# Optimization experiments

Hardware: AMD Instinct MI355X
Metric: run time of the kernel (lower is better)

## Reference

```python
import jax, jax.numpy as jnp
from jax import lax
import numpy as np

EPS = 1e-5
NH = 16  # attention heads (c // 16 with c = 256)


def _qconv(x, mod, phase, padding=0, groups=1):
    """Quaternion conv: real weight = modulus * cos(phase), applied per quaternion component.
    x: (B, C, Q, H, W) -> (B, O, Q, H, W)"""
    w = mod * jnp.cos(phase)
    B, C, Qd, H, W = x.shape
    xr = jnp.transpose(x, (0, 2, 1, 3, 4)).reshape(B * Qd, C, H, W)
    y = lax.conv_general_dilated(xr, w, (1, 1), [(padding, padding)] * 2,
                                 dimension_numbers=('NCHW', 'OIHW', 'NCHW'),
                                 feature_group_count=groups)
    O, Ho, Wo = y.shape[1], y.shape[2], y.shape[3]
    return jnp.transpose(y.reshape(B, Qd, O, Ho, Wo), (0, 2, 1, 3, 4))


def _bn(x):
    # IQBN/VQBN: per-channel normalization over (batch, quaternion, spatial), no affine
    m = x.mean(axis=(0, 2, 3, 4), keepdims=True)
    v = x.var(axis=(0, 2, 3, 4), keepdims=True)
    return (x - m) * lax.rsqrt(v + EPS)


def _attn(x, qkv_m, qkv_p, aproj_m, aproj_p, pe_m, pe_p):
    # QAttention: per-component multi-head self-attention over spatial tokens
    B, C, Qd, H, W = x.shape
    kd = C // NH
    qkv = _qconv(x, qkv_m, qkv_p)  # (B, 3C, Q, H, W)
    q, k, v = jnp.split(qkv, 3, axis=1)
    q = q.reshape(B, NH, kd, Qd, H * W)
    k = k.reshape(B, NH, kd, Qd, H * W)
    v = v.reshape(B, NH, kd, Qd, H * W)
    scores = jnp.einsum('bhcqn,bhcqm->bhqnm', q, k) * (kd ** -0.5)
    a = jax.nn.softmax(scores, axis=-1)
    out = jnp.einsum('bhqnm,bhdqm->bhdqn', a, v).reshape(B, C, Qd, H, W)
    # proj + depthwise positional conv on the input
    return _qconv(out, aproj_m, aproj_p) + _qconv(x, pe_m, pe_p, padding=1, groups=C)


def _psa(x, qkv_m, qkv_p, aproj_m, aproj_p, pe_m, pe_p, ffn1_m, ffn1_p, ffn2_m, ffn2_p):
    a = _attn(x, qkv_m, qkv_p, aproj_m, aproj_p, pe_m, pe_p) + x  # attn shortcut
    h = jax.nn.relu(_bn(_qconv(a, ffn1_m, ffn1_p)))
    f = _bn(_qconv(h, ffn2_m, ffn2_p))
    return f + a  # ffn shortcut


def _msab(x, guide, ec_m, ec_p, gl_w, gl_b, mproj_m, mproj_p):
    # MaxSigmoidAttnBlock (nh=1): global sigmoid gate per (batch, quaternion component)
    B, C, Qd, H, W = x.shape
    e = jax.nn.relu(_bn(_qconv(x, ec_m, ec_p)))  # (B, ec, Q, H, W)
    g = guide @ gl_w.T + gl_b                     # (B, ec)
    ec = g.shape[-1]
    a = jnp.einsum('bcqhw,bc->bq', e, g) / jnp.sqrt(jnp.asarray(ec * H * W, jnp.float32))
    a = jax.nn.sigmoid(a)  # scale param = 1.0 (scale=False)
    e = e * a[:, None, :, None, None]
    return jax.nn.relu(_bn(_qconv(e, mproj_m, mproj_p, padding=1)))


def _forward(x, guide, cv1_m, cv1_p, qkv_m, qkv_p, aproj_m, aproj_p, pe_m, pe_p,
             ffn1_m, ffn1_p, ffn2_m, ffn2_p, ec_m, ec_p, gl_w, gl_b,
             mproj_m, mproj_p, cv2_m, cv2_p):
    y = jax.nn.relu(_bn(_qconv(x, cv1_m, cv1_p)))       # (B, 2c, Q, H, W)
    a, b = jnp.split(y, 2, axis=1)                       # each (B, c, Q, H, W)
    p = _psa(b, qkv_m, qkv_p, aproj_m, aproj_p, pe_m, pe_p,
             ffn1_m, ffn1_p, ffn2_m, ffn2_p)
    m = _msab(p, guide, ec_m, ec_p, gl_w, gl_b, mproj_m, mproj_p)
    cat = jnp.concatenate([a, b, p, m], axis=1)          # (B, 4c, Q, H, W)
    return jax.nn.relu(_bn(_qconv(cat, cv2_m, cv2_p)))   # (B, c2, Q, H, W)


def setup_inputs():
    B, C1, Qd, H, W = 2, 512, 4, 24, 24
    c = 256; ecd = 128; gc = 512; C2 = 512
    ks = jax.random.split(jax.random.key(0), 24)
    def rp(k, shape, s=0.02):
        return s * jax.random.normal(k, shape, dtype=jnp.float32)
    return {
        'x': jax.random.normal(ks[0], (B, C1, Qd, H, W), dtype=jnp.float32),
        'guide': jax.random.normal(ks[1], (B, gc), dtype=jnp.float32),
        'cv1_m': rp(ks[2], (2 * c, C1, 1, 1)),
        'cv1_p': rp(ks[3], (2 * c, C1, 1, 1), 0.1),
        'qkv_m': rp(ks[4], (3 * c, c, 1, 1)),
        'qkv_p': rp(ks[5], (3 * c, c, 1, 1), 0.1),
        'aproj_m': rp(ks[6], (c, c, 1, 1)),
        'aproj_p': rp(ks[7], (c, c, 1, 1), 0.1),
        'pe_m': rp(ks[8], (c, 1, 3, 3)),
        'pe_p': rp(ks[9], (c, 1, 3, 3), 0.1),
        'ffn1_m': rp(ks[10], (2 * c, c, 1, 1)),
        'ffn1_p': rp(ks[11], (2 * c, c, 1, 1), 0.1),
        'ffn2_m': rp(ks[12], (c, 2 * c, 1, 1)),
        'ffn2_p': rp(ks[13], (c, 2 * c, 1, 1), 0.1),
        'ec_m': rp(ks[14], (ecd, c, 1, 1)),
        'ec_p': rp(ks[15], (ecd, c, 1, 1), 0.1),
        'gl_w': rp(ks[16], (ecd, gc), 0.05),
        'gl_b': jnp.zeros((ecd,), dtype=jnp.float32),
        'mproj_m': rp(ks[17], (c, ecd, 3, 3)),
        'mproj_p': rp(ks[18], (c, ecd, 3, 3), 0.1),
        'cv2_m': rp(ks[19], (C2, 4 * c, 1, 1)),
        'cv2_p': rp(ks[20], (C2, 4 * c, 1, 1), 0.1),
    }


def reference(x, guide, cv1_m, cv1_p, qkv_m, qkv_p, aproj_m, aproj_p, pe_m, pe_p,
              ffn1_m, ffn1_p, ffn2_m, ffn2_p, ec_m, ec_p, gl_w, gl_b,
              mproj_m, mproj_p, cv2_m, cv2_p):
    return _forward(x, guide, cv1_m, cv1_p, qkv_m, qkv_p, aproj_m, aproj_p, pe_m, pe_p,
                    ffn1_m, ffn1_p, ffn2_m, ffn2_p, ec_m, ec_p, gl_w, gl_b,
                    mproj_m, mproj_p, cv2_m, cv2_p)
```

## Files before the change

kernel.cpp:

```cpp
#include <hip/hip_runtime.h>
#include <math.h>

typedef __bf16 bf16x8 __attribute__((ext_vector_type(8)));
typedef float f32x4 __attribute__((ext_vector_type(4)));
typedef unsigned short u16;
typedef unsigned int u32;

__device__ __forceinline__ u16 f2bf(float f) {
  u32 u = __float_as_uint(f);
  u32 r = u + 0x7FFF + ((u >> 16) & 1);
  return (u16)(r >> 16);
}
__device__ __forceinline__ float bf2f(u16 h) { return __uint_as_float(((u32)h) << 16); }

static constexpr size_t OB_WBF = 0;
static constexpr size_t OB_WPE = 3276800;
static constexpr size_t OB_ST  = 3286016;
static constexpr size_t OB_GV  = 3310592;
static constexpr size_t OB_GACC= 3311616;
static constexpr size_t OB_CAT = 3311872;
static constexpr size_t OB_YA  = OB_CAT + 9437184;
static constexpr size_t OB_U1  = OB_YA + 9437184;
static constexpr size_t OB_U2  = OB_U1 + 4718592;
static constexpr size_t OB_U3  = OB_U2 + 14155776;
static constexpr size_t OB_AOB = OB_U3 + 4718592;
static constexpr size_t OB_A1B = OB_AOB + 2359296;
static constexpr size_t WS_TOTAL = OB_A1B + 2359296;

struct WPrepP {
  const float* m[8]; const float* p[8];
  u16* out; const float* pem; const float* pep; float* peout;
  int cum[9];
};
__global__ __launch_bounds__(256) void k_wprep(WPrepP P) {
  int i = blockIdx.x * 256 + threadIdx.x;
  if (i < 2304) P.peout[i] = P.pem[i] * cosf(P.pep[i]);
  if (i >= P.cum[8]) return;
  int s = 0;
  while (s < 7 && i >= P.cum[s + 1]) s++;
  int j = i - P.cum[s];
  int src = j;
  if (s == 6) {
    int o = j / 1152, r = j % 1152, kk = r >> 7, cc = r & 127;
    src = (o * 128 + cc) * 9 + kk;
  }
  P.out[i] = f2bf(P.m[s][src] * cosf(P.p[s][src]));
}

__global__ __launch_bounds__(256) void k_xpose(const float* x, u16* xb) {
  int bid = blockIdx.x;
  int mt = bid % 18; bid /= 18;
  int ct = bid % 16; bid /= 16;
  int q = bid & 3, b = bid >> 2;
  __shared__ float tile[32][33];
  int tj = threadIdx.x & 31, ti = threadIdx.x >> 5;
  const float* xp = x + (((size_t)(b * 512 + ct * 32) * 4 + q) * 576) + mt * 32;
#pragma unroll
  for (int ii = 0; ii < 4; ii++)
    tile[ti + ii * 8][tj] = xp[(size_t)(ti + ii * 8) * 4 * 576 + tj];
  __syncthreads();
  u16* yp = xb + ((size_t)b * 2304 + q * 576 + mt * 32) * 512 + ct * 32;
#pragma unroll
  for (int mm = 0; mm < 4; mm++)
    yp[(size_t)(mm * 8 + ti) * 512 + tj] = f2bf(tile[tj][mm * 8 + ti]);
}

struct GemmP {
  const u16* W; const u16* X; float* Y; const float* Add; u16* Yb; float* St;
  long long xOff[8];
  int lda, O, K, M, G;
};

template <int BM, int NWO, int WO, int WM>
__global__ __launch_bounds__(256) void k_gemm(GemmP P) {
  constexpr int FO = WO / 16, FM = WM / 16;
  __shared__ __align__(16) char lds[16384 + BM * 128];
  const int mt = P.M / BM;
  const int ot = P.O >> 7;
  int bid = blockIdx.x;
  const int g = bid / (mt * ot);
  const int rr = bid % (mt * ot);
  const int ob = (rr / mt) << 7;
  const int mb = (rr % mt) * BM;
  const int t = threadIdx.x, lane = t & 63, wave = t >> 6;
  const int wo = (wave % NWO) * WO, wm = (wave / NWO) * WM;
  const u16* Wp = P.W + (size_t)ob * P.K;
  const u16* Xp = P.X + P.xOff[g] + (size_t)mb * P.lda;

  f32x4 acc[FO][FM] = {};

  for (int k0 = 0; k0 < P.K; k0 += 64) {
#pragma unroll
    for (int i = 0; i < 4; i++) {
      int s = (i * 4 + wave) * 64 + lane;
      int row = s >> 3;
      int kg = (s & 7) ^ (row & 7);
      const u16* src = Wp + (size_t)row * P.K + k0 + kg * 8;
      __builtin_amdgcn_global_load_lds(
          (const __attribute__((address_space(1))) u32*)src,
          (__attribute__((address_space(3))) u32*)(lds + (size_t)(i * 4 + wave) * 1024),
          16, 0, 0);
    }
#pragma unroll
    for (int i = 0; i < BM * 8 / 256; i++) {
      int s = (i * 4 + wave) * 64 + lane;
      int row = s >> 3;
      int kg = (s & 7) ^ (row & 7);
      const u16* src = Xp + (size_t)row * P.lda + k0 + kg * 8;
      __builtin_amdgcn_global_load_lds(
          (const __attribute__((address_space(1))) u32*)src,
          (__attribute__((address_space(3))) u32*)(lds + 16384 + (size_t)(i * 4 + wave) * 1024),
          16, 0, 0);
    }
    __syncthreads();
#pragma unroll
    for (int kk = 0; kk < 2; kk++) {
      int kgl = kk * 4 + (lane >> 4);
      bf16x8 af[FO], bfm[FM];
#pragma unroll
      for (int fo = 0; fo < FO; fo++) {
        int row = wo + fo * 16 + (lane & 15);
        af[fo] = *(bf16x8*)&lds[((row << 3) + (kgl ^ (row & 7))) << 4];
      }
#pragma unroll
      for (int fm = 0; fm < FM; fm++) {
        int row = wm + fm * 16 + (lane & 15);
        bfm[fm] = *(bf16x8*)&lds[16384 + (((row << 3) + (kgl ^ (row & 7))) << 4)];
      }
#pragma unroll
      for (int fo = 0; fo < FO; fo++)
#pragma unroll
        for (int fm = 0; fm < FM; fm++)
          acc[fo][fm] = __builtin_amdgcn_mfma_f32_16x16x32_bf16(af[fo], bfm[fm], acc[fo][fm], 0, 0, 0);
    }
    __syncthreads();
  }

  size_t ybase = (size_t)g * P.M * P.O;
#pragma unroll
  for (int fo = 0; fo < FO; fo++) {
    int ow = ob + wo + fo * 16 + ((lane >> 4) << 2);
#pragma unroll
    for (int fm = 0; fm < FM; fm++) {
      int m = mb + wm + fm * 16 + (lane & 15);
      f32x4 v = acc[fo][fm];
      size_t off = ybase + (size_t)m * P.O + ow;
      if (P.Add) v += *(const f32x4*)&P.Add[off];
      if (P.Y) *(f32x4*)&P.Y[off] = v;
      if (P.Yb) {
        ushort4 r;
        r.x = f2bf(v[0]); r.y = f2bf(v[1]); r.z = f2bf(v[2]); r.w = f2bf(v[3]);
        *(ushort4*)&P.Yb[off] = r;
      }
    }
  }

  if (P.St) {
#pragma unroll
    for (int fo = 0; fo < FO; fo++) {
      float sv[4], qv[4];
#pragma unroll
      for (int j = 0; j < 4; j++) { sv[j] = 0.f; qv[j] = 0.f; }
#pragma unroll
      for (int fm = 0; fm < FM; fm++)
#pragma unroll
        for (int j = 0; j < 4; j++) {
          float a = acc[fo][fm][j];
          sv[j] += a;
          qv[j] = fmaf(a, a, qv[j]);
        }
#pragma unroll
      for (int j = 0; j < 4; j++) {
#pragma unroll
        for (int mk = 1; mk < 16; mk <<= 1) {
          sv[j] += __shfl_xor(sv[j], mk, 64);
          qv[j] += __shfl_xor(qv[j], mk, 64);
        }
      }
      if ((lane & 15) == 0) {
        int o = ob + wo + fo * 16 + ((lane >> 4) << 2);
#pragma unroll
        for (int j = 0; j < 4; j++) {
          atomicAdd(&P.St[2 * (o + j)], sv[j]);
          atomicAdd(&P.St[2 * (o + j) + 1], qv[j]);
        }
      }
    }
  }
}

struct NormP {
  const float* X; const float* st; const float* Add;
  u16* Yb; float* Yf; const float* gv; float* gacc;
  long long ybOff[8];
  int ldyb, O, G, M, relu;
  float n;
};
__global__ __launch_bounds__(256) void k_norm(NormP P) {
  int O4 = P.O >> 2;
  long long idx = (long long)blockIdx.x * 256 + threadIdx.x;
  if (idx >= (long long)P.G * P.M * O4) return;
  int c4 = (int)(idx % O4);
  long long gm = idx / O4;
  int m = (int)(gm % P.M);
  int g = (int)(gm / P.M);
  size_t off = (size_t)gm * P.O + c4 * 4;
  f32x4 v = *(const f32x4*)&P.X[off];
  float inv_n = 1.0f / P.n;
#pragma unroll
  for (int j = 0; j < 4; j++) {
    int c = c4 * 4 + j;
    float mean = P.st[2 * c] * inv_n;
    float var = P.st[2 * c + 1] * inv_n - mean * mean;
    v[j] = (v[j] - mean) * rsqrtf(var + 1e-5f);
  }
  if (P.Add) v += *(const f32x4*)&P.Add[off];
  if (P.relu) {
#pragma unroll
    for (int j = 0; j < 4; j++) v[j] = fmaxf(v[j], 0.f);
  }
  if (P.Yb) {
    ushort4 r;
    r.x = f2bf(v[0]); r.y = f2bf(v[1]); r.z = f2bf(v[2]); r.w = f2bf(v[3]);
    *(ushort4*)(P.Yb + P.ybOff[g] + (size_t)m * P.ldyb + c4 * 4) = r;
  }
  if (P.Yf) *(f32x4*)&P.Yf[off] = v;
  if (P.gacc) {
    float gs = 0.f;
#pragma unroll
    for (int j = 0; j < 4; j++) gs = fmaf(v[j], P.gv[g * 128 + c4 * 4 + j], gs);
#pragma unroll
    for (int mk = 1; mk < 64; mk <<= 1) gs += __shfl_xor(gs, mk, 64);
    __shared__ float t1[4];
    int lane = threadIdx.x & 63, wv = threadIdx.x >> 6;
    if (lane == 0) t1[wv] = gs;
    __syncthreads();
    if (threadIdx.x == 0)
      atomicAdd(&P.gacc[g * 4 + m / 576], t1[0] + t1[1] + t1[2] + t1[3]);
  }
}

__global__ __launch_bounds__(256) void k_normT(const float* X, const float* st, float* out) {
  int idx = blockIdx.x * 256 + threadIdx.x;
  if (idx >= 2 * 512 * 576) return;
  int m4 = idx % 576;
  int bo = idx / 576;
  int o = bo & 511, b = bo >> 9;
  float inv_n = 1.0f / 4608.0f;
  float mean = st[2 * o] * inv_n;
  float var = st[2 * o + 1] * inv_n - mean * mean;
  float rs = rsqrtf(var + 1e-5f);
  f32x4 v;
#pragma unroll
  for (int j = 0; j < 4; j++) {
    float x = X[((size_t)b * 2304 + m4 * 4 + j) * 512 + o];
    v[j] = fmaxf((x - mean) * rs, 0.f);
  }
  *(f32x4*)&out[(size_t)bo * 2304 + m4 * 4] = v;
}

__global__ __launch_bounds__(256) void k_pe(const u16* catb, const float* wpe, float* rf) {
  int idx = blockIdx.x * 256 + threadIdx.x;
  if (idx >= 2 * 2304 * 64) return;
  int c4 = idx & 63;
  int gm = idx >> 6;
  int m = gm % 2304, g = gm / 2304;
  int q = m / 576, hw = m % 576, h = hw / 24, w = hw % 24;
  const u16* base = catb + (size_t)g * 2304 * 1024 + 256 + c4 * 4;
  float acc[4];
  {
    ushort4 cv = *(const ushort4*)(base + (size_t)m * 1024);
    acc[0] = bf2f(cv.x); acc[1] = bf2f(cv.y); acc[2] = bf2f(cv.z); acc[3] = bf2f(cv.w);
  }
#pragma unroll
  for (int kh = 0; kh < 3; kh++) {
    int hh = h + kh - 1;
    if (hh < 0 || hh > 23) continue;
#pragma unroll
    for (int kw = 0; kw < 3; kw++) {
      int ww = w + kw - 1;
      if (ww < 0 || ww > 23) continue;
      ushort4 cv = *(const ushort4*)(base + (size_t)(q * 576 + hh * 24 + ww) * 1024);
      float tap[4] = {bf2f(cv.x), bf2f(cv.y), bf2f(cv.z), bf2f(cv.w)};
#pragma unroll
      for (int j = 0; j < 4; j++)
        acc[j] = fmaf(wpe[(c4 * 4 + j) * 9 + kh * 3 + kw], tap[j], acc[j]);
    }
  }
  f32x4 v = {acc[0], acc[1], acc[2], acc[3]};
  *(f32x4*)&rf[(size_t)gm * 256 + c4 * 4] = v;
}

__global__ __launch_bounds__(256) void k_attn(const u16* qkv, u16* ao) {
  int bid = blockIdx.x;
  int tq = bid % 3; int u = bid / 3;
  int qd = u & 3; u >>= 2;
  int head = u & 15, b = u >> 4;
  int t = threadIdx.x, lane = t & 63, wv = t >> 6;
  int g = lane >> 4, q = lane & 15;
  size_t tok0 = (size_t)b * 2304 + qd * 576;
  const u16* QKV = qkv + tok0 * 768;

  __shared__ __align__(16) char shm[50176];
  u16* Kl = (u16*)(shm);
  u16* VT = (u16*)(shm + 27648);
  u16* Pl = (u16*)(shm + 46080 + wv * 1024);

  for (int i = t; i < 1152; i += 256) {
    int m = i >> 1, half = i & 1;
    const u16* src = QKV + (size_t)m * 768 + 256 + head * 16 + half * 8;
    u16 tmp[8];
    *(uint4*)tmp = *(const uint4*)src;
    ushort4 lo, hi;
    lo.x = f2bf(bf2f(tmp[0]) * 0.25f); lo.y = f2bf(bf2f(tmp[1]) * 0.25f);
    lo.z = f2bf(bf2f(tmp[2]) * 0.25f); lo.w = f2bf(bf2f(tmp[3]) * 0.25f);
    hi.x = f2bf(bf2f(tmp[4]) * 0.25f); hi.y = f2bf(bf2f(tmp[5]) * 0.25f);
    hi.z = f2bf(bf2f(tmp[6]) * 0.25f); hi.w = f2bf(bf2f(tmp[7]) * 0.25f);
    u16* dst = Kl + m * 24 + half * 8;
    *(ushort4*)dst = lo;
    *(ushort4*)(dst + 4) = hi;
  }
  for (int mm = t; mm < 576; mm += 256) {
    const u16* src = QKV + (size_t)mm * 768 + 512 + head * 16;
    u16 tmp[16];
    *(uint4*)tmp = *(const uint4*)src;
    *(uint4*)(tmp + 8) = *(const uint4*)(src + 8);
    u16* dst = VT + (mm >> 3) * 128 + (mm & 7);
#pragma unroll
    for (int d = 0; d < 16; d++) dst[d * 8] = tmp[d];
  }
  __syncthreads();

#pragma unroll 1
  for (int i = 0; i < 3; i++) {
    int tl = wv * 3 + i;
    int qbase = tq * 192 + tl * 16;
    bf16x8 qf = {};
    if (g < 2)
      qf = *(const bf16x8*)(QKV + (size_t)(qbase + q) * 768 + head * 16 + g * 8);

    f32x4 acc_o = {};
    float ssum = 0.f;

    for (int ch = 0; ch < 18; ch++) {
      int m0 = ch * 32;
      f32x4 s[2];
#pragma unroll
      for (int h = 0; h < 2; h++) {
        bf16x8 kf = {};
        if (g < 2)
          kf = *(const bf16x8*)(Kl + (size_t)(m0 + h * 16 + q) * 24 + g * 8);
        f32x4 z = {};
        s[h] = __builtin_amdgcn_mfma_f32_16x16x32_bf16(kf, qf, z, 0, 0, 0);
      }
#pragma unroll
      for (int h = 0; h < 2; h++) {
        float p0 = __expf(s[h][0]);
        float p1 = __expf(s[h][1]);
        float p2 = __expf(s[h][2]);
        float p3 = __expf(s[h][3]);
        ssum += (p0 + p1) + (p2 + p3);
        ushort4 w;
        w.x = f2bf(p0); w.y = f2bf(p1); w.z = f2bf(p2); w.w = f2bf(p3);
        *(ushort4*)(Pl + ((h * 2 + (g >> 1)) * 16 + q) * 8 + (g & 1) * 4) = w;
      }
      bf16x8 va = *(const bf16x8*)(VT + ((m0 >> 3) + g) * 128 + q * 8);
      bf16x8 pa = *(const bf16x8*)(Pl + (g * 16 + q) * 8);
      acc_o = __builtin_amdgcn_mfma_f32_16x16x32_bf16(va, pa, acc_o, 0, 0, 0);
    }

    ssum += __shfl_xor(ssum, 16, 64);
    ssum += __shfl_xor(ssum, 32, 64);
    float inv = 1.f / ssum;
    u16* op = ao + (tok0 + qbase + q) * 256 + head * 16 + g * 4;
    ushort4 r;
    r.x = f2bf(acc_o[0] * inv);
    r.y = f2bf(acc_o[1] * inv);
    r.z = f2bf(acc_o[2] * inv);
    r.w = f2bf(acc_o[3] * inv);
    *(ushort4*)op = r;
  }
}

__global__ __launch_bounds__(64) void k_guide(const float* guide, const float* glw,
                                              const float* glb, float* g) {
  int be = blockIdx.x;
  int b = be >> 7, e = be & 127;
  const float* gr = guide + b * 512;
  const float* wr = glw + e * 512;
  float s = 0.f;
  for (int c = threadIdx.x; c < 512; c += 64) s = fmaf(gr[c], wr[c], s);
#pragma unroll
  for (int off = 32; off > 0; off >>= 1) s += __shfl_down(s, off, 64);
  if (threadIdx.x == 0) g[be] = s + glb[e];
}

__global__ __launch_bounds__(256) void k_im2col(const float* ef, const float* gacc, u16* col) {
  int idx = blockIdx.x * 256 + threadIdx.x;
  if (idx >= 8 * 576 * 9) return;
  int kk = idx % 9;
  int gn = idx / 9;
  int n = gn % 576, g = gn / 576;
  int b = g >> 2, q = g & 3;
  int h = n / 24 + kk / 3 - 1, w = n % 24 + kk % 3 - 1;
  u16* cp = col + (size_t)gn * 1152 + kk * 128;
  if (h < 0 || h > 23 || w < 0 || w > 23) {
    ushort4 z = {0, 0, 0, 0};
#pragma unroll
    for (int c4 = 0; c4 < 32; c4++) *(ushort4*)&cp[c4 * 4] = z;
    return;
  }
  float a = gacc[g] / sqrtf(73728.0f);
  float gt = 1.f / (1.f + expf(-a));
  const float* ep = ef + ((size_t)b * 2304 + q * 576 + h * 24 + w) * 128;
  for (int c4 = 0; c4 < 32; c4++) {
    f32x4 v = *(const f32x4*)&ep[c4 * 4];
    ushort4 r;
    r.x = f2bf(v[0] * gt); r.y = f2bf(v[1] * gt);
    r.z = f2bf(v[2] * gt); r.w = f2bf(v[3] * gt);
    *(ushort4*)&cp[c4 * 4] = r;
  }
}

extern "C" void kernel_launch(void* const* d_in, const int* in_sizes, int n_in,
                              void* d_out, int out_size, void* d_ws, size_t ws_size,
                              hipStream_t stream) {
  if (ws_size < WS_TOTAL) return;
  char* ws = (char*)d_ws;
  u16* WB = (u16*)(ws + OB_WBF);
  float* WPE = (float*)(ws + OB_WPE);
  float* STB = (float*)(ws + OB_ST);
  float* GV = (float*)(ws + OB_GV);
  float* GACC = (float*)(ws + OB_GACC);
  u16* CATB = (u16*)(ws + OB_CAT);
  float* YA = (float*)(ws + OB_YA);
  u16* XBF = (u16*)(ws + OB_U1);
  float* A1F = (float*)(ws + OB_U1);
  u16* QKVB = (u16*)(ws + OB_U2);
  u16* COLB = (u16*)(ws + OB_U2);
  float* EF = (float*)(ws + OB_U2 + 10616832);
  float* RF = (float*)(ws + OB_U3);
  u16* HB = (u16*)(ws + OB_U3);
  u16* AOB = (u16*)(ws + OB_AOB);
  u16* A1B = (u16*)(ws + OB_A1B);
  float* out = (float*)d_out;
  const float* x = (const float*)d_in[0];
  const float* guide = (const float*)d_in[1];
  const float* glw = (const float*)d_in[16];
  const float* glb = (const float*)d_in[17];

  hipMemsetAsync(ws + OB_ST, 0, OB_CAT - OB_ST, stream);

  {
    WPrepP p;
    const int mi[8] = {2, 4, 6, 10, 12, 14, 18, 20};
    const int sz[8] = {262144, 196608, 65536, 131072, 131072, 32768, 294912, 524288};
    int c = 0;
    for (int i = 0; i < 8; i++) {
      p.m[i] = (const float*)d_in[mi[i]];
      p.p[i] = (const float*)d_in[mi[i] + 1];
      p.cum[i] = c;
      c += sz[i];
    }
    p.cum[8] = c;
    p.out = WB;
    p.pem = (const float*)d_in[8];
    p.pep = (const float*)d_in[9];
    p.peout = WPE;
    k_wprep<<<(c + 255) / 256, 256, 0, stream>>>(p);
  }
  k_guide<<<256, 64, 0, stream>>>(guide, glw, glb, GV);
  k_xpose<<<2304, 256, 0, stream>>>(x, XBF);

  auto gemm = [&](size_t wOff, int O, int K, int M, int G,
                  const u16* X, long long xs, long long xadd, int lda,
                  float* Y, const float* Add, u16* Yb, int si) {
    GemmP p;
    p.W = WB + wOff; p.X = X; p.Y = Y; p.Add = Add; p.Yb = Yb;
    p.St = (si >= 0) ? (STB + si * 1024) : nullptr;
    p.lda = lda; p.O = O; p.K = K; p.M = M; p.G = G;
    for (int g = 0; g < 8; g++) p.xOff[g] = (long long)(g < G ? g : 0) * xs + xadd;
    int grid = G * (O / 128) * (M / 64);
    k_gemm<64, 4, 32, 64><<<grid, 256, 0, stream>>>(p);
  };
  auto norm = [&](const float* X, int si, int O, int G, int M, const float* Add,
                  u16* Yb, int ldyb, const long long* ybOff, float* Yf, int relu,
                  const float* gv, float* gacc) {
    NormP p;
    p.X = X; p.st = STB + si * 1024; p.Add = Add; p.Yb = Yb; p.Yf = Yf;
    p.gv = gv; p.gacc = gacc;
    p.ldyb = ldyb; p.O = O; p.G = G; p.M = M; p.relu = relu;
    p.n = (float)(G * M);
    for (int g = 0; g < 8; g++) p.ybOff[g] = ybOff ? ybOff[(g < G) ? g : 0] : 0;
    long long total = (long long)G * M * (O / 4);
    k_norm<<<(int)((total + 255) / 256), 256, 0, stream>>>(p);
  };

  gemm(0, 512, 512, 2304, 2, XBF, 2304LL * 512, 0, 512, YA, nullptr, nullptr, 0);
  { long long yo[2] = {0, 2304LL * 1024};
    norm(YA, 0, 512, 2, 2304, nullptr, CATB, 1024, yo, nullptr, 1, nullptr, nullptr); }

  gemm(262144, 768, 256, 2304, 2, CATB, 2304LL * 1024, 256, 1024, nullptr, nullptr, QKVB, -1);
  k_attn<<<384, 256, 0, stream>>>(QKVB, AOB);
  k_pe<<<1152, 256, 0, stream>>>(CATB, WPE, RF);
  gemm(458752, 256, 256, 2304, 2, AOB, 2304LL * 256, 0, 256, A1F, RF, A1B, -1);

  gemm(524288, 512, 256, 2304, 2, A1B, 2304LL * 256, 0, 256, YA, nullptr, nullptr, 1);
  { long long yo[2] = {0, 2304LL * 512};
    norm(YA, 1, 512, 2, 2304, nullptr, HB, 512, yo, nullptr, 1, nullptr, nullptr); }

  gemm(655360, 256, 512, 2304, 2, HB, 2304LL * 512, 0, 512, YA, nullptr, nullptr, 2);
  { long long yo[2] = {512, 2304LL * 1024 + 512};
    norm(YA, 2, 256, 2, 2304, A1F, CATB, 1024, yo, nullptr, 0, nullptr, nullptr); }

  gemm(786432, 128, 256, 2304, 2, CATB, 2304LL * 1024, 512, 1024, YA, nullptr, nullptr, 3);
  norm(YA, 3, 128, 2, 2304, nullptr, nullptr, 0, nullptr, EF, 1, GV, GACC);

  k_im2col<<<162, 256, 0, stream>>>(EF, GACC, COLB);

  gemm(819200, 256, 1152, 576, 8, COLB, 576LL * 1152, 0, 1152, YA, nullptr, nullptr, 4);
  { long long yo[8];
    for (int g = 0; g < 8; g++)
      yo[g] = (long long)(g >> 2) * 2304 * 1024 + (long long)(g & 3) * 576 * 1024 + 768;
    norm(YA, 4, 256, 8, 576, nullptr, CATB, 1024, yo, nullptr, 1, nullptr, nullptr); }

  gemm(1114112, 512, 1024, 2304, 2, CATB, 2304LL * 1024, 0, 1024, YA, nullptr, nullptr, 5);
  k_normT<<<2304, 256, 0, stream>>>(YA, STB + 5 * 1024, out);
}
```

Baseline: 294.8 us.

## Fuse prep kernels, pe conv into proj GEMM, im2col into GEMM, tiled normT

Merges weight prep, input transpose and guide linear into one head kernel. Folds the depthwise positional conv and its residual into the attention projection GEMM epilogue, and builds the gated im2col tile directly in the GEMM's LDS load path. The FFN shortcut now reads the bf16 A1 copy instead of an fp32 buffer, and the final normalize-transpose uses an LDS tile so stores are coalesced. This cuts launches and intermediate memory traffic. The costs are less precision on the residual and heavier GEMM epilogues.

Result: faster. 273.0 us (-7.4%).

```diff
diff --git a/kernel.cpp b/kernel.cpp
--- a/kernel.cpp
+++ b/kernel.cpp
@@ -27,51 +27,73 @@
 static constexpr size_t OB_A1B = OB_AOB + 2359296;
 static constexpr size_t WS_TOTAL = OB_A1B + 2359296;
 
-struct WPrepP {
-  const float* m[8]; const float* p[8];
-  u16* out; const float* pem; const float* pep; float* peout;
-  int cum[9];
+struct HeadP {
+  const float* m[8]; const float* p[8]; u16* wout;
+  const float* pem; const float* pep; float* peout;
+  const float* x; u16* xb;
+  const float* guide; const float* glw; const float* glb; float* gv;
+  int cum[9]; int nwp;
 };
-__global__ __launch_bounds__(256) void k_wprep(WPrepP P) {
-  int i = blockIdx.x * 256 + threadIdx.x;
-  if (i < 2304) P.peout[i] = P.pem[i] * cosf(P.pep[i]);
-  if (i >= P.cum[8]) return;
-  int s = 0;
-  while (s < 7 && i >= P.cum[s + 1]) s++;
-  int j = i - P.cum[s];
-  int src = j;
-  if (s == 6) {
-    int o = j / 1152, r = j % 1152, kk = r >> 7, cc = r & 127;
-    src = (o * 128 + cc) * 9 + kk;
-  }
-  P.out[i] = f2bf(P.m[s][src] * cosf(P.p[s][src]));
-}
-
-__global__ __launch_bounds__(256) void k_xpose(const float* x, u16* xb) {
+__global__ __launch_bounds__(256) void k_head(HeadP P) {
   int bid = blockIdx.x;
-  int mt = bid % 18; bid /= 18;
-  int ct = bid % 16; bid /= 16;
-  int q = bid & 3, b = bid >> 2;
-  __shared__ float tile[32][33];
-  int tj = threadIdx.x & 31, ti = threadIdx.x >> 5;
-  const float* xp = x + (((size_t)(b * 512 + ct * 32) * 4 + q) * 576) + mt * 32;
-#pragma unroll
-  for (int ii = 0; ii < 4; ii++)
-    tile[ti + ii * 8][tj] = xp[(size_t)(ti + ii * 8) * 4 * 576 + tj];
-  __syncthreads();
-  u16* yp = xb + ((size_t)b * 2304 + q * 576 + mt * 32) * 512 + ct * 32;
-#pragma unroll
-  for (int mm = 0; mm < 4; mm++)
-    yp[(size_t)(mm * 8 + ti) * 512 + tj] = f2bf(tile[tj][mm * 8 + ti]);
+  if (bid < P.nwp) {
+    int i = bid * 256 + threadIdx.x;
+    if (i < 2304) {
+      int tap = i >> 8, c = i & 255;
+      P.peout[i] = P.pem[c * 9 + tap] * cosf(P.pep[c * 9 + tap]);
+    }
+    if (i >= P.cum[8]) return;
+    int s = 0;
+    while (s < 7 && i >= P.cum[s + 1]) s++;
+    int j = i - P.cum[s];
+    int src = j;
+    if (s == 6) {
+      int o = j / 1152, r = j % 1152, kk = r >> 7, cc = r & 127;
+      src = (o * 128 + cc) * 9 + kk;
+    }
+    P.wout[i] = f2bf(P.m[s][src] * cosf(P.p[s][src]));
+    return;
+  }
+  bid -= P.nwp;
+  if (bid < 2304) {
+    int mt = bid % 18; bid /= 18;
+    int ct = bid % 16; bid /= 16;
+    int q = bid & 3, b = bid >> 2;
+    __shared__ float tile[32][33];
+    int tj = threadIdx.x & 31, ti = threadIdx.x >> 5;
+    const float* xp = P.x + (((size_t)(b * 512 + ct * 32) * 4 + q) * 576) + mt * 32;
+#pragma unroll
+    for (int ii = 0; ii < 4; ii++)
+      tile[ti + ii * 8][tj] = xp[(size_t)(ti + ii * 8) * 4 * 576 + tj];
+    __syncthreads();
+    u16* yp = P.xb + ((size_t)b * 2304 + q * 576 + mt * 32) * 512 + ct * 32;
+#pragma unroll
+    for (int mm = 0; mm < 4; mm++)
+      yp[(size_t)(mm * 8 + ti) * 512 + tj] = f2bf(tile[tj][mm * 8 + ti]);
+    return;
+  }
+  bid -= 2304;
+  int wv = threadIdx.x >> 6, lane = threadIdx.x & 63;
+  int be = bid * 4 + wv;
+  int b = be >> 7, e = be & 127;
+  const float* gr = P.guide + b * 512;
+  const float* wr = P.glw + e * 512;
+  float s = 0.f;
+  for (int c = lane; c < 512; c += 64) s = fmaf(gr[c], wr[c], s);
+#pragma unroll
+  for (int off = 32; off > 0; off >>= 1) s += __shfl_down(s, off, 64);
+  if (lane == 0) P.gv[be] = s + P.glb[e];
 }
 
 struct GemmP {
-  const u16* W; const u16* X; float* Y; const float* Add; u16* Yb; float* St;
+  const u16* W; const u16* X; float* Y; u16* Yb; float* St;
+  const u16* CAT; const float* W9;
+  const float* EF; const float* GA;
   long long xOff[8];
   int lda, O, K, M, G;
 };
 
-template <int BM, int NWO, int WO, int WM>
+template <int BM, int NWO, int WO, int WM, int MODE>
 __global__ __launch_bounds__(256) void k_gemm(GemmP P) {
   constexpr int FO = WO / 16, FM = WM / 16;
   __shared__ __align__(16) char lds[16384 + BM * 128];
@@ -85,7 +107,15 @@
   const int t = threadIdx.x, lane = t & 63, wave = t >> 6;
   const int wo = (wave % NWO) * WO, wm = (wave / NWO) * WM;
   const u16* Wp = P.W + (size_t)ob * P.K;
-  const u16* Xp = P.X + P.xOff[g] + (size_t)mb * P.lda;
+  const u16* Xp = (MODE == 2) ? nullptr : (P.X + P.xOff[g] + (size_t)mb * P.lda);
+
+  float gt = 0.f;
+  int bq2304 = 0;
+  if constexpr (MODE == 2) {
+    bq2304 = (g >> 2) * 2304 + (g & 3) * 576;
+    float a = P.GA[g] / sqrtf(73728.0f);
+    gt = 1.f / (1.f + __expf(-a));
+  }
 
   f32x4 acc[FO][FM] = {};
 
@@ -101,16 +131,43 @@
           (__attribute__((address_space(3))) u32*)(lds + (size_t)(i * 4 + wave) * 1024),
           16, 0, 0);
     }
-#pragma unroll
-    for (int i = 0; i < BM * 8 / 256; i++) {
-      int s = (i * 4 + wave) * 64 + lane;
-      int row = s >> 3;
-      int kg = (s & 7) ^ (row & 7);
-      const u16* src = Xp + (size_t)row * P.lda + k0 + kg * 8;
-      __builtin_amdgcn_global_load_lds(
-          (const __attribute__((address_space(1))) u32*)src,
-          (__attribute__((address_space(3))) u32*)(lds + 16384 + (size_t)(i * 4 + wave) * 1024),
-          16, 0, 0);
+    if constexpr (MODE != 2) {
+#pragma unroll
+      for (int i = 0; i < BM * 8 / 256; i++) {
+        int s = (i * 4 + wave) * 64 + lane;
+        int row = s >> 3;
+        int kg = (s & 7) ^ (row & 7);
+        const u16* src = Xp + (size_t)row * P.lda + k0 + kg * 8;
+        __builtin_amdgcn_global_load_lds(
+            (const __attribute__((address_space(1))) u32*)src,
+            (__attribute__((address_space(3))) u32*)(lds + 16384 + (size_t)(i * 4 + wave) * 1024),
+            16, 0, 0);
+      }
+    } else {
+#pragma unroll
+      for (int i = 0; i < 2; i++) {
+        int s = t + i * 256;
+        int row = s >> 3, kg = s & 7;
+        int k = k0 + kg * 8;
+        int kk = k >> 7, cc = k & 127;
+        int n = mb + row;
+        int h = n / 24 + kk / 3 - 1, w = n % 24 + kk % 3 - 1;
+        u16 pk[8];
+        if (h >= 0 && h < 24 && w >= 0 && w < 24) {
+          const float* ep = P.EF + ((size_t)(bq2304 + h * 24 + w)) * 128 + cc;
+          f32x4 v0 = *(const f32x4*)ep;
+          f32x4 v1 = *(const f32x4*)(ep + 4);
+#pragma unroll
+          for (int j = 0; j < 4; j++) {
+            pk[j] = f2bf(v0[j] * gt);
+            pk[4 + j] = f2bf(v1[j] * gt);
+          }
+        } else {
+#pragma unroll
+          for (int j = 0; j < 8; j++) pk[j] = 0;
+        }
+        *(uint4*)&lds[16384 + (((row << 3) + (kg ^ (row & 7))) << 4)] = *(uint4*)pk;
+      }
     }
     __syncthreads();
 #pragma unroll
@@ -144,8 +201,26 @@
     for (int fm = 0; fm < FM; fm++) {
       int m = mb + wm + fm * 16 + (lane & 15);
       f32x4 v = acc[fo][fm];
+      if constexpr (MODE == 1) {
+        size_t tokc = ((size_t)g * 2304 + m) * 1024 + 256 + ow;
+        ushort4 cv = *(const ushort4*)&P.CAT[tokc];
+        v[0] += bf2f(cv.x); v[1] += bf2f(cv.y); v[2] += bf2f(cv.z); v[3] += bf2f(cv.w);
+        int q_ = m / 576, hw_ = m % 576, h_ = hw_ / 24, w_ = hw_ % 24;
+        size_t rowb = ((size_t)g * 2304 + q_ * 576) * 1024 + 256 + ow;
+#pragma unroll
+        for (int tp = 0; tp < 9; tp++) {
+          int hh = h_ + tp / 3 - 1, ww = w_ + tp % 3 - 1;
+          if (hh < 0 || hh > 23 || ww < 0 || ww > 23) continue;
+          ushort4 tv = *(const ushort4*)&P.CAT[rowb + (size_t)(hh * 24 + ww) * 1024];
+          f32x4 wt = *(const f32x4*)&P.W9[tp * 256 + ow];
+          v[0] = fmaf(wt[0], bf2f(tv.x), v[0]);
+          v[1] = fmaf(wt[1], bf2f(tv.y), v[1]);
+          v[2] = fmaf(wt[2], bf2f(tv.z), v[2]);
+          v[3] = fmaf(wt[3], bf2f(tv.w), v[3]);
+        }
+        acc[fo][fm] = v;
+      }
       size_t off = ybase + (size_t)m * P.O + ow;
-      if (P.Add) v += *(const f32x4*)&P.Add[off];
       if (P.Y) *(f32x4*)&P.Y[off] = v;
       if (P.Yb) {
         ushort4 r;
@@ -190,7 +265,7 @@
 }
 
 struct NormP {
-  const float* X; const float* st; const float* Add;
+  const float* X; const float* st; const u16* AddB;
   u16* Yb; float* Yf; const float* gv; float* gacc;
   long long ybOff[8];
   int ldyb, O, G, M, relu;
@@ -214,7 +289,10 @@
     float var = P.st[2 * c + 1] * inv_n - mean * mean;
     v[j] = (v[j] - mean) * rsqrtf(var + 1e-5f);
   }
-  if (P.Add) v += *(const f32x4*)&P.Add[off];
+  if (P.AddB) {
+    ushort4 av = *(const ushort4*)(P.AddB + off);
+    v[0] += bf2f(av.x); v[1] += bf2f(av.y); v[2] += bf2f(av.z); v[3] += bf2f(av.w);
+  }
   if (P.relu) {
 #pragma unroll
     for (int j = 0; j < 4; j++) v[j] = fmaxf(v[j], 0.f);
@@ -241,54 +319,29 @@
 }
 
 __global__ __launch_bounds__(256) void k_normT(const float* X, const float* st, float* out) {
-  int idx = blockIdx.x * 256 + threadIdx.x;
-  if (idx >= 2 * 512 * 576) return;
-  int m4 = idx % 576;
-  int bo = idx / 576;
-  int o = bo & 511, b = bo >> 9;
+  int bid = blockIdx.x;
+  int ot = bid & 15;
+  int mt = (bid >> 4) % 72;
+  int b = bid / 1152;
+  int mb = mt * 32, ob = ot * 32;
+  __shared__ float tile[32][33];
+  int c = threadIdx.x & 31, r = threadIdx.x >> 5;
+#pragma unroll
+  for (int i = 0; i < 4; i++) {
+    int row = r + i * 8;
+    tile[row][c] = X[((size_t)b * 2304 + mb + row) * 512 + ob + c];
+  }
+  __syncthreads();
   float inv_n = 1.0f / 4608.0f;
-  float mean = st[2 * o] * inv_n;
-  float var = st[2 * o + 1] * inv_n - mean * mean;
-  float rs = rsqrtf(var + 1e-5f);
-  f32x4 v;
-#pragma unroll
-  for (int j = 0; j < 4; j++) {
-    float x = X[((size_t)b * 2304 + m4 * 4 + j) * 512 + o];
-    v[j] = fmaxf((x - mean) * rs, 0.f);
-  }
-  *(f32x4*)&out[(size_t)bo * 2304 + m4 * 4] = v;
-}
-
-__global__ __launch_bounds__(256) void k_pe(const u16* catb, const float* wpe, float* rf) {
-  int idx = blockIdx.x * 256 + threadIdx.x;
-  if (idx >= 2 * 2304 * 64) return;
-  int c4 = idx & 63;
-  int gm = idx >> 6;
-  int m = gm % 2304, g = gm / 2304;
-  int q = m / 576, hw = m % 576, h = hw / 24, w = hw % 24;
-  const u16* base = catb + (size_t)g * 2304 * 1024 + 256 + c4 * 4;
-  float acc[4];
-  {
-    ushort4 cv = *(const ushort4*)(base + (size_t)m * 1024);
-    acc[0] = bf2f(cv.x); acc[1] = bf2f(cv.y); acc[2] = bf2f(cv.z); acc[3] = bf2f(cv.w);
-  }
-#pragma unroll
-  for (int kh = 0; kh < 3; kh++) {
-    int hh = h + kh - 1;
-    if (hh < 0 || hh > 23) continue;
-#pragma unroll
-    for (int kw = 0; kw < 3; kw++) {
-      int ww = w + kw - 1;
-      if (ww < 0 || ww > 23) continue;
-      ushort4 cv = *(const ushort4*)(base + (size_t)(q * 576 + hh * 24 + ww) * 1024);
-      float tap[4] = {bf2f(cv.x), bf2f(cv.y), bf2f(cv.z), bf2f(cv.w)};
-#pragma unroll
-      for (int j = 0; j < 4; j++)
-        acc[j] = fmaf(wpe[(c4 * 4 + j) * 9 + kh * 3 + kw], tap[j], acc[j]);
-    }
-  }
-  f32x4 v = {acc[0], acc[1], acc[2], acc[3]};
-  *(f32x4*)&rf[(size_t)gm * 256 + c4 * 4] = v;
+#pragma unroll
+  for (int i = 0; i < 4; i++) {
+    int o = ob + r + i * 8;
+    float mean = st[2 * o] * inv_n;
+    float var = st[2 * o + 1] * inv_n - mean * mean;
+    float rs = rsqrtf(var + 1e-5f);
+    float v = fmaxf((tile[c][r + i * 8] - mean) * rs, 0.f);
+    out[((size_t)(b * 512 + o)) * 2304 + mb + c] = v;
+  }
 }
 
 __global__ __launch_bounds__(256) void k_attn(const u16* qkv, u16* ao) {
@@ -382,46 +435,6 @@
   }
 }
 
-__global__ __launch_bounds__(64) void k_guide(const float* guide, const float* glw,
-                                              const float* glb, float* g) {
-  int be = blockIdx.x;
-  int b = be >> 7, e = be & 127;
-  const float* gr = guide + b * 512;
-  const float* wr = glw + e * 512;
-  float s = 0.f;
-  for (int c = threadIdx.x; c < 512; c += 64) s = fmaf(gr[c], wr[c], s);
-#pragma unroll
-  for (int off = 32; off > 0; off >>= 1) s += __shfl_down(s, off, 64);
-  if (threadIdx.x == 0) g[be] = s + glb[e];
-}
-
-__global__ __launch_bounds__(256) void k_im2col(const float* ef, const float* gacc, u16* col) {
-  int idx = blockIdx.x * 256 + threadIdx.x;
-  if (idx >= 8 * 576 * 9) return;
-  int kk = idx % 9;
-  int gn = idx / 9;
-  int n = gn % 576, g = gn / 576;
-  int b = g >> 2, q = g & 3;
-  int h = n / 24 + kk / 3 - 1, w = n % 24 + kk % 3 - 1;
-  u16* cp = col + (size_t)gn * 1152 + kk * 128;
-  if (h < 0 || h > 23 || w < 0 || w > 23) {
-    ushort4 z = {0, 0, 0, 0};
-#pragma unroll
-    for (int c4 = 0; c4 < 32; c4++) *(ushort4*)&cp[c4 * 4] = z;
-    return;
-  }
-  float a = gacc[g] / sqrtf(73728.0f);
-  float gt = 1.f / (1.f + expf(-a));
-  const float* ep = ef + ((size_t)b * 2304 + q * 576 + h * 24 + w) * 128;
-  for (int c4 = 0; c4 < 32; c4++) {
-    f32x4 v = *(const f32x4*)&ep[c4 * 4];
-    ushort4 r;
-    r.x = f2bf(v[0] * gt); r.y = f2bf(v[1] * gt);
-    r.z = f2bf(v[2] * gt); r.w = f2bf(v[3] * gt);
-    *(ushort4*)&cp[c4 * 4] = r;
-  }
-}
-
 extern "C" void kernel_launch(void* const* d_in, const int* in_sizes, int n_in,
                               void* d_out, int out_size, void* d_ws, size_t ws_size,
                               hipStream_t stream) {
@@ -435,24 +448,17 @@
   u16* CATB = (u16*)(ws + OB_CAT);
   float* YA = (float*)(ws + OB_YA);
   u16* XBF = (u16*)(ws + OB_U1);
-  float* A1F = (float*)(ws + OB_U1);
   u16* QKVB = (u16*)(ws + OB_U2);
-  u16* COLB = (u16*)(ws + OB_U2);
   float* EF = (float*)(ws + OB_U2 + 10616832);
-  float* RF = (float*)(ws + OB_U3);
   u16* HB = (u16*)(ws + OB_U3);
   u16* AOB = (u16*)(ws + OB_AOB);
   u16* A1B = (u16*)(ws + OB_A1B);
   float* out = (float*)d_out;
-  const float* x = (const float*)d_in[0];
-  const float* guide = (const float*)d_in[1];
-  const float* glw = (const float*)d_in[16];
-  const float* glb = (const float*)d_in[17];
 
   hipMemsetAsync(ws + OB_ST, 0, OB_CAT - OB_ST, stream);
 
   {
-    WPrepP p;
+    HeadP p;
     const int mi[8] = {2, 4, 6, 10, 12, 14, 18, 20};
     const int sz[8] = {262144, 196608, 65536, 131072, 131072, 32768, 294912, 524288};
     int c = 0;
@@ -463,31 +469,43 @@
       c += sz[i];
     }
     p.cum[8] = c;
-    p.out = WB;
+    p.wout = WB;
     p.pem = (const float*)d_in[8];
     p.pep = (const float*)d_in[9];
     p.peout = WPE;
-    k_wprep<<<(c + 255) / 256, 256, 0, stream>>>(p);
-  }
-  k_guide<<<256, 64, 0, stream>>>(guide, glw, glb, GV);
-  k_xpose<<<2304, 256, 0, stream>>>(x, XBF);
-
-  auto gemm = [&](size_t wOff, int O, int K, int M, int G,
+    p.x = (const float*)d_in[0];
+    p.xb = XBF;
+    p.guide = (const float*)d_in[1];
+    p.glw = (const float*)d_in[16];
+    p.glb = (const float*)d_in[17];
+    p.gv = GV;
+    p.nwp = (c + 255) / 256;
+    int grid = p.nwp + 2304 + 64;
+    k_head<<<grid, 256, 0, stream>>>(p);
+  }
+
+  auto gemm = [&](int mode, size_t wOff, int O, int K, int M, int G,
                   const u16* X, long long xs, long long xadd, int lda,
-                  float* Y, const float* Add, u16* Yb, int si) {
+                  float* Y, u16* Yb, int si) {
     GemmP p;
-    p.W = WB + wOff; p.X = X; p.Y = Y; p.Add = Add; p.Yb = Yb;
+    p.W = WB + wOff; p.X = X; p.Y = Y; p.Yb = Yb;
     p.St = (si >= 0) ? (STB + si * 1024) : nullptr;
+    p.CAT = CATB; p.W9 = WPE; p.EF = EF; p.GA = GACC;
     p.lda = lda; p.O = O; p.K = K; p.M = M; p.G = G;
     for (int g = 0; g < 8; g++) p.xOff[g] = (long long)(g < G ? g : 0) * xs + xadd;
     int grid = G * (O / 128) * (M / 64);
-    k_gemm<64, 4, 32, 64><<<grid, 256, 0, stream>>>(p);
+    if (mode == 0)
+      k_gemm<64, 4, 32, 64, 0><<<grid, 256, 0, stream>>>(p);
+    else if (mode == 1)
+      k_gemm<64, 4, 32, 64, 1><<<grid, 256, 0, stream>>>(p);
+    else
+      k_gemm<64, 4, 32, 64, 2><<<grid, 256, 0, stream>>>(p);
   };
-  auto norm = [&](const float* X, int si, int O, int G, int M, const float* Add,
+  auto norm = [&](const float* X, int si, int O, int G, int M, const u16* AddB,
                   u16* Yb, int ldyb, const long long* ybOff, float* Yf, int relu,
                   const float* gv, float* gacc) {
     NormP p;
-    p.X = X; p.st = STB + si * 1024; p.Add = Add; p.Yb = Yb; p.Yf = Yf;
+    p.X = X; p.st = STB + si * 1024; p.AddB = AddB; p.Yb = Yb; p.Yf = Yf;
     p.gv = gv; p.gacc = gacc;
     p.ldyb = ldyb; p.O = O; p.G = G; p.M = M; p.relu = relu;
     p.n = (float)(G * M);
@@ -496,34 +514,31 @@
     k_norm<<<(int)((total + 255) / 256), 256, 0, stream>>>(p);
   };
 
-  gemm(0, 512, 512, 2304, 2, XBF, 2304LL * 512, 0, 512, YA, nullptr, nullptr, 0);
+  gemm(0, 0, 512, 512, 2304, 2, XBF, 2304LL * 512, 0, 512, YA, nullptr, 0);
   { long long yo[2] = {0, 2304LL * 1024};
     norm(YA, 0, 512, 2, 2304, nullptr, CATB, 1024, yo, nullptr, 1, nullptr, nullptr); }
 
-  gemm(262144, 768, 256, 2304, 2, CATB, 2304LL * 1024, 256, 1024, nullptr, nullptr, QKVB, -1);
+  gemm(0, 262144, 768, 256, 2304, 2, CATB, 2304LL * 1024, 256, 1024, nullptr, QKVB, -1);
   k_attn<<<384, 256, 0, stream>>>(QKVB, AOB);
-  k_pe<<<1152, 256, 0, stream>>>(CATB, WPE, RF);
-  gemm(458752, 256, 256, 2304, 2, AOB, 2304LL * 256, 0, 256, A1F, RF, A1B, -1);
-
-  gemm(524288, 512, 256, 2304, 2, A1B, 2304LL * 256, 0, 256, YA, nullptr, nullptr, 1);
+  gemm(1, 458752, 256, 256, 2304, 2, AOB, 2304LL * 256, 0, 256, nullptr, A1B, -1);
+
+  gemm(0, 524288, 512, 256, 2304, 2, A1B, 2304LL * 256, 0, 256, YA, nullptr, 1);
   { long long yo[2] = {0, 2304LL * 512};
     norm(YA, 1, 512, 2, 2304, nullptr, HB, 512, yo, nullptr, 1, nullptr, nullptr); }
 
-  gemm(655360, 256, 512, 2304, 2, HB, 2304LL * 512, 0, 512, YA, nullptr, nullptr, 2);
+  gemm(0, 655360, 256, 512, 2304, 2, HB, 2304LL * 512, 0, 512, YA, nullptr, 2);
   { long long yo[2] = {512, 2304LL * 1024 + 512};
-    norm(YA, 2, 256, 2, 2304, A1F, CATB, 1024, yo, nullptr, 0, nullptr, nullptr); }
-
-  gemm(786432, 128, 256, 2304, 2, CATB, 2304LL * 1024, 512, 1024, YA, nullptr, nullptr, 3);
+    norm(YA, 2, 256, 2, 2304, A1B, CATB, 1024, yo, nullptr, 0, nullptr, nullptr); }
+
+  gemm(0, 786432, 128, 256, 2304, 2, CATB, 2304LL * 1024, 512, 1024, YA, nullptr, 3);
   norm(YA, 3, 128, 2, 2304, nullptr, nullptr, 0, nullptr, EF, 1, GV, GACC);
 
-  k_im2col<<<162, 256, 0, stream>>>(EF, GACC, COLB);
-
-  gemm(819200, 256, 1152, 576, 8, COLB, 576LL * 1152, 0, 1152, YA, nullptr, nullptr, 4);
+  gemm(2, 819200, 256, 1152, 576, 8, nullptr, 0, 0, 0, YA, nullptr, 4);
   { long long yo[8];
     for (int g = 0; g < 8; g++)
       yo[g] = (long long)(g >> 2) * 2304 * 1024 + (long long)(g & 3) * 576 * 1024 + 768;
     norm(YA, 4, 256, 8, 576, nullptr, CATB, 1024, yo, nullptr, 1, nullptr, nullptr); }
 
-  gemm(1114112, 512, 1024, 2304, 2, CATB, 2304LL * 1024, 0, 1024, YA, nullptr, nullptr, 5);
+  gemm(0, 1114112, 512, 1024, 2304, 2, CATB, 2304LL * 1024, 0, 1024, YA, nullptr, 5);
   k_normT<<<2304, 256, 0, stream>>>(YA, STB + 5 * 1024, out);
 }
```
